# Optimization experiments

Measured on AMD Instinct MI355X. Metric: run time of the kernel, lower is better.

## Reference

```python
import jax, jax.numpy as jnp
import numpy as np

B, T, C, H = 2, 2048, 1024, 16
HD = C // H
MAX_WAVELENGTH = 10000.0


def apply_rope(x, positions):
    # x: [B, H, T, HD], positions: [T]
    fraction = 2.0 * jnp.arange(HD // 2, dtype=jnp.float32) / HD
    timescale = MAX_WAVELENGTH ** fraction  # [HD//2]
    sinusoid = positions[:, None] / timescale[None, :]  # [T, HD//2]
    sin = jnp.sin(sinusoid)
    cos = jnp.cos(sinusoid)
    first, second = jnp.split(x, 2, axis=-1)
    out = jnp.concatenate(
        [first * cos - second * sin, second * cos + first * sin], axis=-1
    )
    return out.astype(x.dtype)


def setup_inputs() -> dict:
    key = jax.random.key(0)
    k1, k2, k3 = jax.random.split(key, 3)
    x = jax.random.normal(k1, (B, T, C), dtype=jnp.float32)
    w_attn = jax.random.normal(k2, (C, 3 * C), dtype=jnp.float32) * 0.02
    b_attn = jnp.zeros((3 * C,), dtype=jnp.float32)
    w_proj = jax.random.normal(k3, (C, C), dtype=jnp.float32) * 0.02
    b_proj = jnp.zeros((C,), dtype=jnp.float32)
    return {"x": x, "w_attn": w_attn, "b_attn": b_attn,
            "w_proj": w_proj, "b_proj": b_proj}


def reference(x, w_attn, b_attn, w_proj, b_proj):
    b, t, c = x.shape
    qkv = x @ w_attn + b_attn  # [B, T, 3C]
    q, k, v = jnp.split(qkv, 3, axis=-1)
    q = q.reshape(b, t, H, HD).transpose(0, 2, 1, 3)  # [B, H, T, HD]
    k = k.reshape(b, t, H, HD).transpose(0, 2, 1, 3)
    v = v.reshape(b, t, H, HD).transpose(0, 2, 1, 3)
    positions = jnp.arange(t, dtype=x.dtype)
    q = apply_rope(q, positions)
    k = apply_rope(k, positions)
    att = jnp.einsum('bhqd,bhkd->bhqk', q, k) * (1.0 / jnp.sqrt(HD))
    causal = jnp.tril(jnp.ones((t, t), dtype=bool))
    att = jnp.where(causal, att, jnp.finfo(att.dtype).min)
    att = jax.nn.softmax(att, axis=-1)
    y = jnp.einsum('bhqk,bhkd->bhqd', att, v)
    y = y.transpose(0, 2, 1, 3).reshape(b, t, c)
    return y @ w_proj + b_proj
```

## Files before the change

### kernel.cpp

```cpp
#include <hip/hip_runtime.h>
#include <hip/hip_bf16.h>


typedef __attribute__((ext_vector_type(8))) short short8;
typedef __attribute__((ext_vector_type(4))) float floatx4;

__device__ __forceinline__ unsigned short f2bf(float f) {
    union { float f; unsigned int u; } v; v.f = f;
    unsigned int r = v.u + 0x7FFFu + ((v.u >> 16) & 1u);
    return (unsigned short)(r >> 16);
}

__device__ __forceinline__ unsigned int pk2bf(float a, float b) {
    union { float f; unsigned int u; } ua, ub;
    ua.f = a; ub.f = b;
    return __builtin_amdgcn_perm(ub.u + 0x8000u, ua.u + 0x8000u, 0x07060302u);
}

__device__ __forceinline__ unsigned int cvtpk(float a, float b) {
    unsigned int r;
    asm("v_cvt_pk_bf16_f32 %0, %1, %2" : "=v"(r) : "v"(a), "v"(b));
    return r;
}

__device__ __forceinline__ void gld16(const void* g, void* l) {
    __builtin_amdgcn_global_load_lds(
        (const __attribute__((address_space(1))) unsigned int*)g,
        (__attribute__((address_space(3))) unsigned int*)l, 16, 0, 0);
}

__device__ __forceinline__ void transpose_body(
    const float* __restrict__ in, unsigned short* __restrict__ out,
    int R, int NC, int bx, int by, int tid,
    unsigned short (*tile)[68]) {
    int r0 = by * 64, c0 = bx * 64;
    int c4 = (tid & 15) * 4, rr = tid >> 4;
#pragma unroll
    for (int i = 0; i < 4; i++) {
        int row = rr + i * 16;
        float4 v = *(const float4*)&in[(size_t)(r0 + row) * NC + c0 + c4];
        ushort4 o;
        o.x = f2bf(v.x); o.y = f2bf(v.y); o.z = f2bf(v.z); o.w = f2bf(v.w);
        *(ushort4*)&tile[row][c4] = o;
    }
    __syncthreads();
    int col = tid & 63, rr2 = tid >> 6;
#pragma unroll
    for (int i = 0; i < 16; i++) {
        int orow = rr2 + i * 4;
        out[(size_t)(c0 + orow) * R + r0 + col] = tile[col][orow];
    }
}

__global__ __launch_bounds__(256) void prep(
    const float* __restrict__ x,
    const float* __restrict__ w_attn,
    const float* __restrict__ w_proj,
    unsigned short* __restrict__ x_bf,
    unsigned short* __restrict__ wTa,
    unsigned short* __restrict__ wTp,
    float2* __restrict__ tab) {
    __shared__ unsigned short tile[64][68];
    int bid = blockIdx.x;
    int tid = threadIdx.x;
    if (bid < 4096) {
        int i = bid * 256 + tid;
        float4 v = ((const float4*)x)[i];
        ushort4 o;
        o.x = f2bf(v.x); o.y = f2bf(v.y); o.z = f2bf(v.z); o.w = f2bf(v.w);
        ((ushort4*)x_bf)[i] = o;
    } else if (bid < 4864) {
        int t = bid - 4096;
        transpose_body(w_attn, wTa, 1024, 3072, t % 48, t / 48, tid, tile);
    } else if (bid < 5120) {
        int t = bid - 4864;
        transpose_body(w_proj, wTp, 1024, 1024, t & 15, t >> 4, tid, tile);
    } else {
        int i = (bid - 5120) * 256 + tid;
        int t = i >> 5, d = i & 31;
        float inv_ts = exp2f(-0.41524101186092036f * (float)d);
        float ang = (float)t * inv_ts;
        tab[i] = make_float2(sinf(ang), cosf(ang));
    }
}

__global__ __launch_bounds__(512) void gemm_qkv(
    const unsigned short* __restrict__ A,
    const unsigned short* __restrict__ BT,
    const float* __restrict__ bias,
    const float2* __restrict__ tab,
    unsigned short* __restrict__ qT,
    unsigned short* __restrict__ kT,
    unsigned short* __restrict__ vT) {
    __shared__ __align__(16) unsigned short smem[32768];
    int tid = threadIdx.x;
    int lane = tid & 63;
    int w = tid >> 6;
    int wx = w & 3, wy = w >> 2;
    int l16 = lane & 15, quad = lane >> 4;
    int lin = blockIdx.x;
    int xcd = lin & 7, idx = lin >> 3;
    int mb = (xcd >> 1) * 8 + idx / 12;
    int nb = (xcd & 1) * 12 + idx % 12;
    int m0 = mb * 128;
    int n0 = nb * 128;
    int x = l16 & 7;
    int lr = lane >> 3;
    int gc = (lane & 7) ^ lr;

    floatx4 acc[4][2];
#pragma unroll
    for (int mi = 0; mi < 4; mi++)
#pragma unroll
        for (int ni = 0; ni < 2; ni++)
            acc[mi][ni] = (floatx4){0.f, 0.f, 0.f, 0.f};

    auto stage = [&](int bsel, int k0) {
        unsigned short* as = smem + bsel * 16384;
        unsigned short* bs = as + 8192;
#pragma unroll
        for (int i = 0; i < 2; i++) {
            int seg = w * 2 + i;
            int row = seg * 8 + lr;
            gld16(A + (size_t)(m0 + row) * 1024 + k0 + gc * 8, &as[seg * 512]);
            gld16(BT + (size_t)(n0 + row) * 1024 + k0 + gc * 8, &bs[seg * 512]);
        }
    };

    auto compute = [&](int bsel) {
        const unsigned short* as = smem + bsel * 16384;
        const unsigned short* bs = as + 8192;
#pragma unroll
        for (int kk = 0; kk < 2; kk++) {
            short8 af[4], bf[2];
#pragma unroll
            for (int mi = 0; mi < 4; mi++) {
                int r = wy * 64 + mi * 16 + l16;
                af[mi] = *(const short8*)&as[r * 64 + (((kk << 2) | quad) ^ x) * 8];
            }
#pragma unroll
            for (int ni = 0; ni < 2; ni++) {
                int r = wx * 32 + ni * 16 + l16;
                bf[ni] = *(const short8*)&bs[r * 64 + (((kk << 2) | quad) ^ x) * 8];
            }
#pragma unroll
            for (int mi = 0; mi < 4; mi++)
#pragma unroll
                for (int ni = 0; ni < 2; ni++)
                    acc[mi][ni] = __builtin_amdgcn_mfma_f32_16x16x32_bf16(
                        af[mi], bf[ni], acc[mi][ni], 0, 0, 0);
        }
    };

    stage(0, 0);
    int cur = 0;
    for (int k0 = 0; k0 < 960; k0 += 64) {
        stage(cur ^ 1, k0 + 64);
        asm volatile("s_waitcnt vmcnt(4)" ::: "memory");
        __builtin_amdgcn_s_barrier();
        compute(cur);
        asm volatile("s_waitcnt lgkmcnt(0)" ::: "memory");
        __builtin_amdgcn_s_barrier();
        cur ^= 1;
    }
    asm volatile("s_waitcnt vmcnt(0)" ::: "memory");
    __builtin_amdgcn_s_barrier();
    compute(cur);
    __syncthreads();

    int region = n0 >> 10;
    int b = m0 >> 11;
    float b0 = bias[n0 + wx * 32 + l16];
    float b1 = bias[n0 + wx * 32 + 16 + l16];

    if (region < 2) {
        unsigned short* qk = region ? kT : qT;
        float scale = region ? 1.0f : 0.18033688011112042f;
        float* F = (float*)smem;
#pragma unroll
        for (int mi = 0; mi < 4; mi++)
#pragma unroll
            for (int ni = 0; ni < 2; ni++) {
                float bv = ni ? b1 : b0;
                int col = wx * 32 + ni * 16 + l16;
#pragma unroll
                for (int r = 0; r < 4; r++) {
                    int row = wy * 64 + mi * 16 + quad * 4 + r;
                    F[row * 128 + (col ^ ((row & 7) << 2))] = acc[mi][ni][r] + bv;
                }
            }
        __syncthreads();
        int tl = tid >> 2, qq = tid & 3;
        int hl = qq >> 1, d0 = (qq & 1) * 16;
        int t = (m0 & 2047) + tl;
        int xr = (tl & 7) << 2;
        unsigned int lo[8], hi[8];
#pragma unroll
        for (int j = 0; j < 8; j++) {
            float o1[2], o2[2];
#pragma unroll
            for (int e = 0; e < 2; e++) {
                int d = d0 + j * 2 + e;
                float v1 = F[tl * 128 + ((hl * 64 + d) ^ xr)];
                float v2 = F[tl * 128 + ((hl * 64 + d + 32) ^ xr)];
                float2 sc = tab[t * 32 + d];
                o1[e] = (v1 * sc.y - v2 * sc.x) * scale;
                o2[e] = (v2 * sc.y + v1 * sc.x) * scale;
            }
            lo[j] = (unsigned int)f2bf(o1[0]) | ((unsigned int)f2bf(o1[1]) << 16);
            hi[j] = (unsigned int)f2bf(o2[0]) | ((unsigned int)f2bf(o2[1]) << 16);
        }
        __syncthreads();
        unsigned short* lq = smem;
        int base = tl * 136 + hl * 64 + d0;
#pragma unroll
        for (int j = 0; j < 4; j++) {
            *(uint2*)&lq[base + 4 * j] = make_uint2(lo[2 * j], lo[2 * j + 1]);
            *(uint2*)&lq[base + 32 + 4 * j] = make_uint2(hi[2 * j], hi[2 * j + 1]);
        }
        __syncthreads();
        int c8 = tid & 7;
        int hl2 = (tid >> 3) & 1;
        int tl0 = tid >> 4;
        int h = ((n0 & 1023) >> 6) + hl2;
        unsigned short* ob = qk + (size_t)(b * 16 + h) * 2048 * 64;
#pragma unroll
        for (int p = 0; p < 4; p++) {
            int tl_ = p * 32 + tl0;
            int tt = (m0 & 2047) + tl_;
            short8 val = *(const short8*)&lq[tl_ * 136 + hl2 * 64 + c8 * 8];
            *(short8*)&ob[(size_t)tt * 64 + c8 * 8] = val;
        }
    } else {
#pragma unroll
        for (int mi = 0; mi < 4; mi++)
#pragma unroll
            for (int ni = 0; ni < 2; ni++) {
                int d_loc = wx * 32 + ni * 16 + l16;
                int t_base = wy * 64 + mi * 16 + quad * 4;
                float bv = ni ? b1 : b0;
                uint2 pk;
                pk.x = pk2bf(acc[mi][ni][0] + bv, acc[mi][ni][1] + bv);
                pk.y = pk2bf(acc[mi][ni][2] + bv, acc[mi][ni][3] + bv);
                int e = d_loc * 128 + (t_base ^ ((d_loc & 15) << 3));
                *(uint2*)&smem[e] = pk;
            }
        __syncthreads();
        int d_r = tid >> 2, qtr = tid & 3;
        int cv = (n0 - 2048) + d_r;
        int hh = cv >> 6, dd = cv & 63;
        int fofs = (d_r & 15) << 3;
        size_t vbase = ((size_t)(b * 16 + hh) * 64 + dd) * 2048 + (m0 & 2047);
#pragma unroll
        for (int c = 0; c < 4; c++) {
            int tc = qtr * 32 + c * 8;
            short8 val = *(const short8*)&smem[d_r * 128 + (tc ^ fofs)];
            *(short8*)&vT[vbase + tc] = val;
        }
    }
}

__global__ __launch_bounds__(256) void gemm_proj(
    const unsigned short* __restrict__ A,
    const unsigned short* __restrict__ BT,
    const float* __restrict__ bias,
    float* __restrict__ out) {
    __shared__ __align__(16) unsigned short smem[24576];
    int lane = threadIdx.x & 63;
    int w = threadIdx.x >> 6;
    int wx = w & 1, wy = w >> 1;
    int l16 = lane & 15, quad = lane >> 4;
    int lin = blockIdx.x;
    int swz = (lin & 7) * 64 + (lin >> 3);
    int m0 = (swz >> 4) * 128;
    int n0 = (swz & 15) * 64;
    int x = l16 & 7;
    int lr = lane >> 3;
    int gc = (lane & 7) ^ lr;

    floatx4 acc[4][2];
#pragma unroll
    for (int mi = 0; mi < 4; mi++)
#pragma unroll
        for (int ni = 0; ni < 2; ni++)
            acc[mi][ni] = (floatx4){0.f, 0.f, 0.f, 0.f};

    auto stage = [&](int bsel, int k0) {
        unsigned short* as = smem + bsel * 12288;
        unsigned short* bs = as + 8192;
#pragma unroll
        for (int i = 0; i < 6; i++) {
            int seg = w * 6 + i;
            if (seg < 16) {
                int row = seg * 8 + lr;
                gld16(A + (size_t)(m0 + row) * 1024 + k0 + gc * 8, &as[seg * 512]);
            } else {
                int s2 = seg - 16;
                int row = s2 * 8 + lr;
                gld16(BT + (size_t)(n0 + row) * 1024 + k0 + gc * 8, &bs[s2 * 512]);
            }
        }
    };

    auto compute = [&](int bsel) {
        const unsigned short* as = smem + bsel * 12288;
        const unsigned short* bs = as + 8192;
#pragma unroll
        for (int kk = 0; kk < 2; kk++) {
            short8 af[4], bf[2];
#pragma unroll
            for (int mi = 0; mi < 4; mi++) {
                int r = wy * 64 + mi * 16 + l16;
                af[mi] = *(const short8*)&as[r * 64 + (((kk << 2) | quad) ^ x) * 8];
            }
#pragma unroll
            for (int ni = 0; ni < 2; ni++) {
                int r = wx * 32 + ni * 16 + l16;
                bf[ni] = *(const short8*)&bs[r * 64 + (((kk << 2) | quad) ^ x) * 8];
            }
#pragma unroll
            for (int mi = 0; mi < 4; mi++)
#pragma unroll
                for (int ni = 0; ni < 2; ni++)
                    acc[mi][ni] = __builtin_amdgcn_mfma_f32_16x16x32_bf16(
                        af[mi], bf[ni], acc[mi][ni], 0, 0, 0);
        }
    };

    stage(0, 0);
    int cur = 0;
    for (int k0 = 0; k0 < 960; k0 += 64) {
        stage(cur ^ 1, k0 + 64);
        asm volatile("s_waitcnt vmcnt(6)" ::: "memory");
        __builtin_amdgcn_s_barrier();
        compute(cur);
        asm volatile("s_waitcnt lgkmcnt(0)" ::: "memory");
        __builtin_amdgcn_s_barrier();
        cur ^= 1;
    }
    asm volatile("s_waitcnt vmcnt(0)" ::: "memory");
    __builtin_amdgcn_s_barrier();
    compute(cur);

#pragma unroll
    for (int mi = 0; mi < 4; mi++)
#pragma unroll
        for (int ni = 0; ni < 2; ni++) {
            int row = m0 + wy * 64 + mi * 16 + quad * 4;
            int col = n0 + wx * 32 + ni * 16 + l16;
            float bv = bias[col];
#pragma unroll
            for (int r = 0; r < 4; r++)
                out[(size_t)(row + r) * 1024 + col] = acc[mi][ni][r] + bv;
        }
}

__global__ __launch_bounds__(256) void attn5(
    const unsigned short* __restrict__ qT,
    const unsigned short* __restrict__ kT,
    const unsigned short* __restrict__ vT,
    unsigned short* __restrict__ y) {
    __shared__ __align__(16) unsigned short kbuf[2][64 * 64];
    __shared__ __align__(16) unsigned short vbuf[2][64 * 64];
    __shared__ __align__(16) unsigned short pl[4][16 * 72];
    int lane = threadIdx.x & 63;
    int w = threadIdx.x >> 6;
    int l16 = lane & 15, quad = lane >> 4;
    int blk = blockIdx.x;
    int t = 31 - (blk >> 5);
    int bh = blk & 31;
    int b = bh >> 4, h = bh & 15;
    int q0 = t * 64 + w * 16;
    const unsigned short* qp = qT + (size_t)bh * 2048 * 64;
    unsigned short* plw = pl[w];
    int x = l16 & 7;

    short8 qf0 = *(const short8*)(qp + (size_t)(q0 + l16) * 64 + quad * 8);
    short8 qf1 = *(const short8*)(qp + (size_t)(q0 + l16) * 64 + 32 + quad * 8);

    short8 ones;
#pragma unroll
    for (int j = 0; j < 8; j++) ones[j] = (short)0x3F80;

    floatx4 acc[4];
#pragma unroll
    for (int ni = 0; ni < 4; ni++) acc[ni] = (floatx4){0.f, 0.f, 0.f, 0.f};
    floatx4 accl = (floatx4){0.f, 0.f, 0.f, 0.f};

    int lr8 = lane >> 3, l8 = lane & 7;
    const unsigned short* sp[4];
    unsigned short* ld0[4];
    int gstep;
    if (w < 2) {
        const unsigned short* kp = kT + (size_t)bh * 2048 * 64;
#pragma unroll
        for (int i = 0; i < 4; i++) {
            int seg = w * 4 + i;
            int row = seg * 8 + lr8;
            int c = l8 ^ (row & 7);
            sp[i] = kp + (size_t)row * 64 + c * 8;
            ld0[i] = &kbuf[0][seg * 512];
        }
        gstep = 4096;
    } else {
        const unsigned short* vp = vT + (size_t)bh * 64 * 2048;
#pragma unroll
        for (int i = 0; i < 4; i++) {
            int s = (w - 2) * 4 + i;
            int d = s * 8 + lr8;
            int c = l8 ^ (d & 7);
            sp[i] = vp + (size_t)d * 2048 + c * 8;
            ld0[i] = &vbuf[0][s * 512];
        }
        gstep = 64;
    }

    auto stage = [&](int bi) {
#pragma unroll
        for (int i = 0; i < 4; i++) {
            gld16(sp[i], ld0[i] + bi * 4096);
            sp[i] += gstep;
        }
    };

    int L = t + 1;
    int query = q0 + l16;
    stage(0);
    int cur = 0;
    for (int it = 0; it < L; it++) {
        if (it + 1 < L) {
            stage(cur ^ 1);
            asm volatile("s_waitcnt vmcnt(4)" ::: "memory");
        } else {
            asm volatile("s_waitcnt vmcnt(0)" ::: "memory");
        }
        __builtin_amdgcn_s_barrier();
        const unsigned short* kb = kbuf[cur];
        const unsigned short* vb = vbuf[cur];
        bool diag = (it == t);
        floatx4 s4[4];
        __builtin_amdgcn_s_setprio(1);
#pragma unroll
        for (int c = 0; c < 4; c++) {
            int r = c * 16 + l16;
            short8 kf0 = *(const short8*)&kb[r * 64 + ((quad) ^ x) * 8];
            short8 kf1 = *(const short8*)&kb[r * 64 + ((quad | 4) ^ x) * 8];
            floatx4 z = (floatx4){0.f, 0.f, 0.f, 0.f};
            z = __builtin_amdgcn_mfma_f32_16x16x32_bf16(kf0, qf0, z, 0, 0, 0);
            z = __builtin_amdgcn_mfma_f32_16x16x32_bf16(kf1, qf1, z, 0, 0, 0);
            s4[c] = z;
        }
        __builtin_amdgcn_s_setprio(0);
        int j0 = it * 64;
#pragma unroll
        for (int c = 0; c < 4; c++) {
            float p[4];
#pragma unroll
            for (int r = 0; r < 4; r++) {
                float e = __builtin_amdgcn_exp2f(s4[c][r]);
                if (diag) {
                    int key = j0 + c * 16 + quad * 4 + r;
                    e = (key <= query) ? e : 0.f;
                }
                p[r] = e;
            }
            uint2 pk;
            pk.x = cvtpk(p[0], p[1]);
            pk.y = cvtpk(p[2], p[3]);
            *(uint2*)&plw[l16 * 72 + c * 16 + quad * 4] = pk;
        }
        short8 pa0 = *(const short8*)&plw[l16 * 72 + quad * 8];
        short8 pa1 = *(const short8*)&plw[l16 * 72 + 32 + quad * 8];
        __builtin_amdgcn_s_setprio(1);
        accl = __builtin_amdgcn_mfma_f32_16x16x32_bf16(pa0, ones, accl, 0, 0, 0);
        accl = __builtin_amdgcn_mfma_f32_16x16x32_bf16(pa1, ones, accl, 0, 0, 0);
#pragma unroll
        for (int ni = 0; ni < 4; ni++) {
            int d = ni * 16 + l16;
            short8 vf0 = *(const short8*)&vb[d * 64 + ((quad) ^ x) * 8];
            short8 vf1 = *(const short8*)&vb[d * 64 + ((quad | 4) ^ x) * 8];
            acc[ni] = __builtin_amdgcn_mfma_f32_16x16x32_bf16(pa0, vf0, acc[ni], 0, 0, 0);
            acc[ni] = __builtin_amdgcn_mfma_f32_16x16x32_bf16(pa1, vf1, acc[ni], 0, 0, 0);
        }
        __builtin_amdgcn_s_setprio(0);
        asm volatile("s_waitcnt lgkmcnt(0)" ::: "memory");
        __builtin_amdgcn_s_barrier();
        cur ^= 1;
    }

    float inv[4];
#pragma unroll
    for (int r = 0; r < 4; r++) inv[r] = 1.f / accl[r];
#pragma unroll
    for (int ni = 0; ni < 4; ni++)
#pragma unroll
        for (int r = 0; r < 4; r++) {
            int tr = q0 + quad * 4 + r;
            y[((size_t)(b * 2048 + tr)) * 1024 + h * 64 + ni * 16 + l16] =
                f2bf(acc[ni][r] * inv[r]);
        }
}

extern "C" void kernel_launch(void* const* d_in, const int* in_sizes, int n_in,
                              void* d_out, int out_size, void* d_ws, size_t ws_size,
                              hipStream_t stream) {
    const float* x      = (const float*)d_in[0];
    const float* w_attn = (const float*)d_in[1];
    const float* b_attn = (const float*)d_in[2];
    const float* w_proj = (const float*)d_in[3];
    const float* b_proj = (const float*)d_in[4];
    float* out = (float*)d_out;

    char* ws = (char*)d_ws;
    unsigned short* x_bf = (unsigned short*)ws;
    unsigned short* wTa  = (unsigned short*)(ws + (8ull << 20));
    unsigned short* wTp  = (unsigned short*)(ws + (14ull << 20));
    unsigned short* qTb  = (unsigned short*)(ws + (16ull << 20));
    unsigned short* kTb  = (unsigned short*)(ws + (24ull << 20));
    unsigned short* vTb  = (unsigned short*)(ws + (32ull << 20));
    float2*         tab  = (float2*)(ws + (40ull << 20));
    unsigned short* y_bf = x_bf;

    prep<<<5376, 256, 0, stream>>>(x, w_attn, w_proj, x_bf, wTa, wTp, tab);
    gemm_qkv<<<768, 512, 0, stream>>>(x_bf, wTa, b_attn, tab, qTb, kTb, vTb);
    attn5<<<1024, 256, 0, stream>>>(qTb, kTb, vTb, y_bf);
    gemm_proj<<<512, 256, 0, stream>>>(y_bf, wTp, b_proj, out);
}
```

Baseline: 162.1 us.

## Widen QKV GEMM tile to 128x384 and emit epilogue per 64-column head group

The QKV GEMM block tile grows from 128x128 to 128x384, so each block reuses its A tile across three times as many columns. The grid drops from 768 to 256 blocks of 512 threads, with 24 accumulators per wave and double the shared memory. The epilogue becomes a loop over six 64-column groups, each doing RoPE, scaling and the Q/K/V layout writes through a transposed padded staging buffer. The trade is less A-tile traffic against fewer blocks for the 256 CUs, higher register pressure, and more barriers in the epilogue.

New measurement: 168.9 us. 1.04x slower.

```diff
diff --git a/kernel.cpp b/kernel.cpp
--- a/kernel.cpp
+++ b/kernel.cpp
@@ -92,61 +92,64 @@
     unsigned short* __restrict__ qT,
     unsigned short* __restrict__ kT,
     unsigned short* __restrict__ vT) {
-    __shared__ __align__(16) unsigned short smem[32768];
+    __shared__ __align__(16) unsigned short smem[65536];
     int tid = threadIdx.x;
     int lane = tid & 63;
     int w = tid >> 6;
     int wx = w & 3, wy = w >> 2;
     int l16 = lane & 15, quad = lane >> 4;
     int lin = blockIdx.x;
-    int xcd = lin & 7, idx = lin >> 3;
-    int mb = (xcd >> 1) * 8 + idx / 12;
-    int nb = (xcd & 1) * 12 + idx % 12;
-    int m0 = mb * 128;
-    int n0 = nb * 128;
+    int m0 = (lin >> 3) * 128;
+    int ng = lin & 7;
+    int n0 = ng * 384;
     int x = l16 & 7;
     int lr = lane >> 3;
     int gc = (lane & 7) ^ lr;
 
-    floatx4 acc[4][2];
+    floatx4 acc[4][6];
 #pragma unroll
     for (int mi = 0; mi < 4; mi++)
 #pragma unroll
-        for (int ni = 0; ni < 2; ni++)
+        for (int ni = 0; ni < 6; ni++)
             acc[mi][ni] = (floatx4){0.f, 0.f, 0.f, 0.f};
 
     auto stage = [&](int bsel, int k0) {
-        unsigned short* as = smem + bsel * 16384;
+        unsigned short* as = smem + bsel * 32768;
         unsigned short* bs = as + 8192;
 #pragma unroll
         for (int i = 0; i < 2; i++) {
             int seg = w * 2 + i;
             int row = seg * 8 + lr;
             gld16(A + (size_t)(m0 + row) * 1024 + k0 + gc * 8, &as[seg * 512]);
+        }
+#pragma unroll
+        for (int i = 0; i < 6; i++) {
+            int seg = w * 6 + i;
+            int row = seg * 8 + lr;
             gld16(BT + (size_t)(n0 + row) * 1024 + k0 + gc * 8, &bs[seg * 512]);
         }
     };
 
     auto compute = [&](int bsel) {
-        const unsigned short* as = smem + bsel * 16384;
+        const unsigned short* as = smem + bsel * 32768;
         const unsigned short* bs = as + 8192;
 #pragma unroll
         for (int kk = 0; kk < 2; kk++) {
-            short8 af[4], bf[2];
+            short8 af[4], bf[6];
 #pragma unroll
             for (int mi = 0; mi < 4; mi++) {
                 int r = wy * 64 + mi * 16 + l16;
                 af[mi] = *(const short8*)&as[r * 64 + (((kk << 2) | quad) ^ x) * 8];
             }
 #pragma unroll
-            for (int ni = 0; ni < 2; ni++) {
-                int r = wx * 32 + ni * 16 + l16;
+            for (int ni = 0; ni < 6; ni++) {
+                int r = wx * 96 + ni * 16 + l16;
                 bf[ni] = *(const short8*)&bs[r * 64 + (((kk << 2) | quad) ^ x) * 8];
             }
 #pragma unroll
             for (int mi = 0; mi < 4; mi++)
 #pragma unroll
-                for (int ni = 0; ni < 2; ni++)
+                for (int ni = 0; ni < 6; ni++)
                     acc[mi][ni] = __builtin_amdgcn_mfma_f32_16x16x32_bf16(
                         af[mi], bf[ni], acc[mi][ni], 0, 0, 0);
         }
@@ -156,7 +159,7 @@
     int cur = 0;
     for (int k0 = 0; k0 < 960; k0 += 64) {
         stage(cur ^ 1, k0 + 64);
-        asm volatile("s_waitcnt vmcnt(4)" ::: "memory");
+        asm volatile("s_waitcnt vmcnt(8)" ::: "memory");
         __builtin_amdgcn_s_barrier();
         compute(cur);
         asm volatile("s_waitcnt lgkmcnt(0)" ::: "memory");
@@ -168,94 +171,112 @@
     compute(cur);
     __syncthreads();
 
-    int region = n0 >> 10;
     int b = m0 >> 11;
-    float b0 = bias[n0 + wx * 32 + l16];
-    float b1 = bias[n0 + wx * 32 + 16 + l16];
-
-    if (region < 2) {
-        unsigned short* qk = region ? kT : qT;
-        float scale = region ? 1.0f : 0.18033688011112042f;
-        float* F = (float*)smem;
-#pragma unroll
-        for (int mi = 0; mi < 4; mi++)
-#pragma unroll
-            for (int ni = 0; ni < 2; ni++) {
-                float bv = ni ? b1 : b0;
-                int col = wx * 32 + ni * 16 + l16;
-#pragma unroll
-                for (int r = 0; r < 4; r++) {
-                    int row = wy * 64 + mi * 16 + quad * 4 + r;
-                    F[row * 128 + (col ^ ((row & 7) << 2))] = acc[mi][ni][r] + bv;
+    float bb[6];
+#pragma unroll
+    for (int ni = 0; ni < 6; ni++)
+        bb[ni] = bias[n0 + wx * 96 + ni * 16 + l16];
+
+    float* F = (float*)smem;
+    unsigned short* U = smem + 16512;
+    unsigned short* V = smem;
+
+    for (int g = 0; g < 6; g++) {
+        int col0 = n0 + g * 64;
+        int region = col0 >> 10;
+        if (region < 2) {
+            unsigned short* qk = region ? kT : qT;
+            float scale = region ? 1.0f : 0.18033688011112042f;
+#pragma unroll
+            for (int mi = 0; mi < 4; mi++)
+#pragma unroll
+                for (int ni = 0; ni < 6; ni++) {
+                    int c = wx * 96 + ni * 16;
+                    if ((c >> 6) == g) {
+                        int dl = c - g * 64 + l16;
+#pragma unroll
+                        for (int r = 0; r < 4; r++) {
+                            int row = wy * 64 + mi * 16 + quad * 4 + r;
+                            F[dl * 129 + row] = acc[mi][ni][r] + bb[ni];
+                        }
+                    }
                 }
-            }
-        __syncthreads();
-        int tl = tid >> 2, qq = tid & 3;
-        int hl = qq >> 1, d0 = (qq & 1) * 16;
-        int t = (m0 & 2047) + tl;
-        int xr = (tl & 7) << 2;
-        unsigned int lo[8], hi[8];
-#pragma unroll
-        for (int j = 0; j < 8; j++) {
-            float o1[2], o2[2];
-#pragma unroll
-            for (int e = 0; e < 2; e++) {
-                int d = d0 + j * 2 + e;
-                float v1 = F[tl * 128 + ((hl * 64 + d) ^ xr)];
-                float v2 = F[tl * 128 + ((hl * 64 + d + 32) ^ xr)];
-                float2 sc = tab[t * 32 + d];
-                o1[e] = (v1 * sc.y - v2 * sc.x) * scale;
-                o2[e] = (v2 * sc.y + v1 * sc.x) * scale;
-            }
-            lo[j] = (unsigned int)f2bf(o1[0]) | ((unsigned int)f2bf(o1[1]) << 16);
-            hi[j] = (unsigned int)f2bf(o2[0]) | ((unsigned int)f2bf(o2[1]) << 16);
-        }
-        __syncthreads();
-        unsigned short* lq = smem;
-        int base = tl * 136 + hl * 64 + d0;
-#pragma unroll
-        for (int j = 0; j < 4; j++) {
-            *(uint2*)&lq[base + 4 * j] = make_uint2(lo[2 * j], lo[2 * j + 1]);
-            *(uint2*)&lq[base + 32 + 4 * j] = make_uint2(hi[2 * j], hi[2 * j + 1]);
-        }
-        __syncthreads();
-        int c8 = tid & 7;
-        int hl2 = (tid >> 3) & 1;
-        int tl0 = tid >> 4;
-        int h = ((n0 & 1023) >> 6) + hl2;
-        unsigned short* ob = qk + (size_t)(b * 16 + h) * 2048 * 64;
-#pragma unroll
-        for (int p = 0; p < 4; p++) {
-            int tl_ = p * 32 + tl0;
-            int tt = (m0 & 2047) + tl_;
-            short8 val = *(const short8*)&lq[tl_ * 136 + hl2 * 64 + c8 * 8];
-            *(short8*)&ob[(size_t)tt * 64 + c8 * 8] = val;
-        }
-    } else {
-#pragma unroll
-        for (int mi = 0; mi < 4; mi++)
-#pragma unroll
-            for (int ni = 0; ni < 2; ni++) {
-                int d_loc = wx * 32 + ni * 16 + l16;
-                int t_base = wy * 64 + mi * 16 + quad * 4;
-                float bv = ni ? b1 : b0;
-                uint2 pk;
-                pk.x = pk2bf(acc[mi][ni][0] + bv, acc[mi][ni][1] + bv);
-                pk.y = pk2bf(acc[mi][ni][2] + bv, acc[mi][ni][3] + bv);
-                int e = d_loc * 128 + (t_base ^ ((d_loc & 15) << 3));
-                *(uint2*)&smem[e] = pk;
-            }
-        __syncthreads();
-        int d_r = tid >> 2, qtr = tid & 3;
-        int cv = (n0 - 2048) + d_r;
-        int hh = cv >> 6, dd = cv & 63;
-        int fofs = (d_r & 15) << 3;
-        size_t vbase = ((size_t)(b * 16 + hh) * 64 + dd) * 2048 + (m0 & 2047);
-#pragma unroll
-        for (int c = 0; c < 4; c++) {
-            int tc = qtr * 32 + c * 8;
-            short8 val = *(const short8*)&smem[d_r * 128 + (tc ^ fofs)];
-            *(short8*)&vT[vbase + tc] = val;
+            __syncthreads();
+            {
+                int tl = tid >> 2, sub = tid & 3;
+                int t = (m0 & 2047) + tl;
+                int d0 = sub * 8;
+                unsigned int lo[4], hi[4];
+#pragma unroll
+                for (int j = 0; j < 8; j += 2) {
+                    float o1[2], o2[2];
+#pragma unroll
+                    for (int e = 0; e < 2; e++) {
+                        int d = d0 + j + e;
+                        float v1 = F[d * 129 + tl];
+                        float v2 = F[(d + 32) * 129 + tl];
+                        float2 sc = tab[t * 32 + d];
+                        o1[e] = (v1 * sc.y - v2 * sc.x) * scale;
+                        o2[e] = (v2 * sc.y + v1 * sc.x) * scale;
+                    }
+                    lo[j >> 1] = (unsigned int)f2bf(o1[0]) |
+                                 ((unsigned int)f2bf(o1[1]) << 16);
+                    hi[j >> 1] = (unsigned int)f2bf(o2[0]) |
+                                 ((unsigned int)f2bf(o2[1]) << 16);
+                }
+                *(uint2*)&U[tl * 72 + d0]          = make_uint2(lo[0], lo[1]);
+                *(uint2*)&U[tl * 72 + d0 + 4]      = make_uint2(lo[2], lo[3]);
+                *(uint2*)&U[tl * 72 + 32 + d0]     = make_uint2(hi[0], hi[1]);
+                *(uint2*)&U[tl * 72 + 32 + d0 + 4] = make_uint2(hi[2], hi[3]);
+            }
+            __syncthreads();
+            {
+                int h = (col0 & 1023) >> 6;
+                unsigned short* ob = qk + (size_t)(b * 16 + h) * 2048 * 64;
+                int rr = tid >> 3;
+                int c8 = tid & 7;
+#pragma unroll
+                for (int p = 0; p < 2; p++) {
+                    int row = rr + p * 64;
+                    int t = (m0 & 2047) + row;
+                    short8 val = *(const short8*)&U[row * 72 + c8 * 8];
+                    *(short8*)&ob[(size_t)t * 64 + c8 * 8] = val;
+                }
+            }
+            __syncthreads();
+        } else {
+#pragma unroll
+            for (int mi = 0; mi < 4; mi++)
+#pragma unroll
+                for (int ni = 0; ni < 6; ni++) {
+                    int c = wx * 96 + ni * 16;
+                    if ((c >> 6) == g) {
+                        int dl = c - g * 64 + l16;
+                        int t_base = wy * 64 + mi * 16 + quad * 4;
+                        float bv = bb[ni];
+                        uint2 pk;
+                        pk.x = pk2bf(acc[mi][ni][0] + bv, acc[mi][ni][1] + bv);
+                        pk.y = pk2bf(acc[mi][ni][2] + bv, acc[mi][ni][3] + bv);
+                        int e = dl * 128 + (t_base ^ ((dl & 15) << 3));
+                        *(uint2*)&V[e] = pk;
+                    }
+                }
+            __syncthreads();
+            {
+                int d_r = tid >> 3;
+                int c8 = tid & 7;
+                int cv = (col0 - 2048) + d_r;
+                int hh = cv >> 6, dd = cv & 63;
+                int fofs = (d_r & 15) << 3;
+                size_t vbase = ((size_t)(b * 16 + hh) * 64 + dd) * 2048 + (m0 & 2047);
+#pragma unroll
+                for (int p = 0; p < 2; p++) {
+                    int tc = c8 * 8 + p * 64;
+                    short8 val = *(const short8*)&V[d_r * 128 + (tc ^ fofs)];
+                    *(short8*)&vT[vbase + tc] = val;
+                }
+            }
+            __syncthreads();
         }
     }
 }
@@ -522,7 +543,7 @@
     unsigned short* y_bf = x_bf;
 
     prep<<<5376, 256, 0, stream>>>(x, w_attn, w_proj, x_bf, wTa, wTp, tab);
-    gemm_qkv<<<768, 512, 0, stream>>>(x_bf, wTa, b_attn, tab, qTb, kTb, vTb);
+    gemm_qkv<<<256, 512, 0, stream>>>(x_bf, wTa, b_attn, tab, qTb, kTb, vTb);
     attn5<<<1024, 256, 0, stream>>>(qTb, kTb, vTb, y_bf);
     gemm_proj<<<512, 256, 0, stream>>>(y_bf, wTp, b_proj, out);
 }
```
